# Kernel optimization log

Hardware: AMD Instinct MI355X
Metric: run time of the kernel (lower is better)

The kernel has to match this reference:

```python
import jax, jax.numpy as jnp
import numpy as np

B, T, D, O = 32, 1024, 1024, 256


def _glorot(key, shape):
    fan_in, fan_out = shape[0], shape[-1]
    std = np.sqrt(2.0 / (fan_in + fan_out))
    return jax.random.normal(key, shape, dtype=jnp.float32) * std


def setup_inputs() -> dict:
    key = jax.random.key(0)
    ks = jax.random.split(key, 14)
    return {
        "inputs": jax.random.normal(ks[0], (B, T, D), dtype=jnp.float32),
        # attention cell params
        "Wa": _glorot(ks[1], (O, O)),
        "Ua": _glorot(ks[2], (D, O)),
        "Va": _glorot(ks[3], (O, 1)),
        "Ba1": _glorot(ks[4], (1, O)),
        "Ba2": _glorot(ks[5], (T, O)),
        "Ba3": _glorot(ks[6], (T, 1)),
        # cascaded GRU cell params (Bo1 and inner keras GRUCell are unused in call)
        "Wo": _glorot(ks[7], (O, 1)),
        "Uo": _glorot(ks[8], (D, O)),
        "Co": _glorot(ks[9], (D, O)),
        "Bo2": _glorot(ks[10], (1, O)),
        "Bo3": _glorot(ks[11], (1, O)),
        "Bo4": _glorot(ks[12], (1, O)),
        "emb": _glorot(ks[13], (O, O)),
    }


def reference(inputs, Wa, Ua, Va, Ba1, Ba2, Ba3, Wo, Uo, Co, Bo2, Bo3, Bo4, emb):
    # inputs: [B, T, D]
    # UaH is identical every decoder step in the original code -> hoist (same math).
    UaH = jnp.einsum("btd,do->bto", inputs, Ua) + Ba2          # [B,T,O]
    # prev_state at step t is inputs[:, t-1, :] with wraparound at t=0.
    prev_in = jnp.roll(inputs, 1, axis=1)                        # [B,T,D]
    UoH_all = jnp.einsum("btd,do->bto", prev_in, Uo) + Bo2      # [B,T,O]

    def step(prev_pred, uoh_t):
        # --- attention cell (query = tanh(prev_pred)) ---
        WaS = jnp.tanh(prev_pred) @ Wa + Ba1                     # [B,O]
        scores = jnp.tanh(UaH + WaS[:, None, :]) @ Va + Ba3     # [B,T,1]
        sm = jax.nn.softmax(scores, axis=1)                      # [B,T,1]
        ctx = jnp.sum(inputs * sm, axis=1)                       # [B,D]
        # --- cascaded GRU cell ---
        woy = (jax.nn.softmax(prev_pred) @ emb) @ Wo             # [B,1]
        coc = ctx @ Co + Bo3                                     # [B,O]
        pred = woy + uoh_t + coc + Bo4                           # [B,O]
        return pred, pred

    init = jnp.zeros((inputs.shape[0], Wa.shape[0]), dtype=inputs.dtype)
    _, outs = jax.lax.scan(step, init, jnp.swapaxes(UoH_all, 0, 1))  # [T,B,O]
    return jnp.swapaxes(outs, 0, 1)                                   # [B,T,O]
```

## Files before the change

### kernel.cpp

```cpp
#include <hip/hip_runtime.h>
#include <hip/hip_fp16.h>


typedef unsigned int uint32;
typedef unsigned short u16;

#define NTH 512

__device__ __forceinline__ float b2f(u16 u) { return __uint_as_float(((uint32)u) << 16); }
__device__ __forceinline__ u16 f2b(float f) {
    uint32 u = __float_as_uint(f);
    uint32 r = u + 0x7fffu + ((u >> 16) & 1u);
    return (u16)(r >> 16);
}
__device__ __forceinline__ float lo_bf(uint32 d) { return __uint_as_float(d << 16); }
__device__ __forceinline__ float hi_bf(uint32 d) { return __uint_as_float(d & 0xffff0000u); }
__device__ __forceinline__ float tanh_fast(float x) {
    float e = __expf(x + x);
    return 1.0f - 2.0f * __builtin_amdgcn_rcpf(e + 1.0f);
}
__device__ __forceinline__ uint32 packh(float f, int t) {
    return (((uint32)t) << 16) | (uint32)__half_as_ushort(__float2half(f));
}
__device__ __forceinline__ float unpackh(uint32 w) {
    return __half2float(__ushort_as_half((unsigned short)(w & 0xFFFFu)));
}

#define OFF_E  ((size_t)0)
#define OFF_IC ((size_t)16777216)
#define WS_NEEDED ((size_t)33554432)

__device__ uint32 g_P[2][32][2064];
__device__ float g_embWo[256];

__global__ __launch_bounds__(256) void init_k() {
    int i = blockIdx.x * 256 + threadIdx.x;
    ((uint32*)g_P)[i] = 0xFFFF0000u;
}

__global__ void setup_embWo(const float* __restrict__ emb, const float* __restrict__ Wo) {
    int o = threadIdx.x;
    float a = 0.f;
    for (int j = 0; j < 256; j++) a = fmaf(emb[o * 256 + j], Wo[j], a);
    g_embWo[o] = a;
}

__global__ __launch_bounds__(256) void gemm_pre(
    const float* __restrict__ in, const float* __restrict__ Ua,
    const float* __restrict__ Uo, const float* __restrict__ Co,
    const float* __restrict__ Ba2, const float* __restrict__ Bo2,
    const float* __restrict__ Bo3, const float* __restrict__ Bo4,
    u16* __restrict__ E, float* __restrict__ outStage, u16* __restrict__ ic) {
    __shared__ __align__(16) float smA[32][132];
    __shared__ __align__(16) float smB[32][128];

    int tid = threadIdx.x;
    int rt = blockIdx.x, ct = blockIdx.y;
    int mat = ct >> 1;
    int o0 = (ct & 1) * 128;
    const float* W = (mat == 0) ? Ua : (mat == 1 ? Uo : Co);
    int r0 = rt * 128;
    int b = r0 >> 10, t0 = r0 & 1023;
    int tr = tid >> 4, tc = tid & 15;

    float acc[8][8];
#pragma unroll
    for (int i = 0; i < 8; i++)
#pragma unroll
        for (int j = 0; j < 8; j++) acc[i][j] = 0.f;

    for (int kc = 0; kc < 1024; kc += 32) {
#pragma unroll
        for (int l = 0; l < 4; l++) {
            int s = tid + l * 256;
            int i = s >> 3, c = s & 7;
            float4 v = *(const float4*)(in + (size_t)(r0 + i) * 1024 + kc + c * 4);
            smA[c * 4 + 0][i] = v.x;
            smA[c * 4 + 1][i] = v.y;
            smA[c * 4 + 2][i] = v.z;
            smA[c * 4 + 3][i] = v.w;
        }
#pragma unroll
        for (int l = 0; l < 4; l++) {
            int s = tid + l * 256;
            int dd = s >> 5, c = s & 31;
            *(float4*)&smB[dd][c * 4] = *(const float4*)(W + (size_t)(kc + dd) * 256 + o0 + c * 4);
        }
        __syncthreads();
#pragma unroll 4
        for (int j = 0; j < 32; j++) {
            float a0[8], b0[8];
            *(float4*)&a0[0] = *(const float4*)&smA[j][tr * 8];
            *(float4*)&a0[4] = *(const float4*)&smA[j][tr * 8 + 4];
            *(float4*)&b0[0] = *(const float4*)&smB[j][tc * 8];
            *(float4*)&b0[4] = *(const float4*)&smB[j][tc * 8 + 4];
#pragma unroll
            for (int rr = 0; rr < 8; rr++)
#pragma unroll
                for (int cc = 0; cc < 8; cc++) acc[rr][cc] = fmaf(a0[rr], b0[cc], acc[rr][cc]);
        }
        __syncthreads();
    }

    if (mat == 0) {
#pragma unroll
        for (int rr = 0; rr < 8; rr++) {
            int t = t0 + tr * 8 + rr;
#pragma unroll
            for (int cc = 0; cc < 8; cc++) {
                int o = o0 + tc * 8 + cc;
                float v = __expf(2.f * (acc[rr][cc] + Ba2[t * 256 + o]));
                E[((((size_t)b << 10) + t) << 8) + o] = f2b(v);
            }
        }
    } else if (mat == 1) {
#pragma unroll
        for (int rr = 0; rr < 8; rr++) {
            int t = t0 + tr * 8 + rr;
            int t1 = (t + 1) & 1023;
#pragma unroll
            for (int cc = 0; cc < 8; cc++) {
                int o = o0 + tc * 8 + cc;
                outStage[(((size_t)b << 10) + t1) * 256 + o] = acc[rr][cc] + Bo2[o] + Bo3[o] + Bo4[o];
            }
        }
    } else {
#pragma unroll
        for (int rr = 0; rr < 8; rr++) {
            int t = t0 + tr * 8 + rr;
#pragma unroll
            for (int cc = 0; cc < 8; cc++)
                ic[(((size_t)b << 10) + t) * 256 + o0 + tc * 8 + cc] = f2b(acc[rr][cc]);
        }
    }
}

__global__ __launch_bounds__(NTH) void seq8(
    const float* __restrict__ Wa, const float* __restrict__ Va,
    const float* __restrict__ Ba1, const float* __restrict__ Ba3,
    const u16* __restrict__ E, const u16* __restrict__ IC,
    float* __restrict__ out) {
    __shared__ uint32 smWa2[128 * 256];
    __shared__ __align__(16) float smScratch[2064];
    __shared__ float smPred[256], smQ[256], smF[256], smVa[256], smBa1[256];
    __shared__ float smS[128], smEe[128], smBa3[128];
    __shared__ float smT[16];

    int tid = threadIdx.x;
    int b = blockIdx.x & 31, g = blockIdx.x >> 5;
    int lane = tid & 63, w = tid >> 6;
    int t0 = g << 7;

    if (tid < 256) {
        smVa[tid] = Va[tid]; smBa1[tid] = Ba1[tid];
        smPred[tid] = 0.f; smQ[tid] = 0.f;
    }
    if (tid < 128) smBa3[tid] = Ba3[t0 + tid];
    for (int idx = tid; idx < 32768; idx += NTH) {
        int j2 = idx >> 8, o = idx & 255;
        uint32 u0 = (uint32)f2b(Wa[(size_t)(2 * j2) * 256 + o]);
        uint32 u1 = (uint32)f2b(Wa[(size_t)(2 * j2 + 1) * 256 + o]);
        smWa2[idx] = u0 | (u1 << 16);
    }
    __syncthreads();

    float sv = (tid < 256) ? smVa[tid] : 0.f;
#pragma unroll
    for (int off = 32; off; off >>= 1) sv += __shfl_xor(sv, off, 64);
    if (lane == 0) smT[w] = sv;
    __syncthreads();
    float sumVa = smT[0] + smT[1] + smT[2] + smT[3];
    float myEmb = (tid < 256) ? g_embWo[tid] : 0.f;
    __syncthreads();

    const u16* Eb = E + ((size_t)b << 18);
    const u16* ICb = IC + ((size_t)b << 18);
    float* outb = out + ((size_t)b << 18);
    long bud = 1000000000L;

    for (int t = 0; t < 1024; t++) {
        uint32* buf = &g_P[t & 1][b][0];
        float uoh = (tid < 256) ? outb[((size_t)t << 8) + tid] : 0.f;

        float pv = 0.f;
        if (tid < 256) {
            pv = smPred[tid];
            float m = pv;
#pragma unroll
            for (int off = 32; off; off >>= 1) m = fmaxf(m, __shfl_xor(m, off, 64));
            if (lane == 0) smT[w] = m;
        }
        {
            int o = tid & 255, h = tid >> 8;
            const uint32* wp = &smWa2[(h << 6) * 256 + o];
            const float* qp = &smQ[h << 7];
            float a = 0.f;
#pragma unroll 8
            for (int j2 = 0; j2 < 64; j2++) {
                float2 q2 = *(const float2*)&qp[j2 * 2];
                uint32 p = wp[j2 << 8];
                a = fmaf(lo_bf(p), q2.x, a);
                a = fmaf(hi_bf(p), q2.y, a);
            }
            smScratch[tid] = a;
        }
        __syncthreads();
        if (tid < 256) {
            float M = fmaxf(fmaxf(smT[0], smT[1]), fmaxf(smT[2], smT[3]));
            float e = __expf(pv - M);
            float s1 = e, s2 = e * myEmb;
#pragma unroll
            for (int off = 32; off; off >>= 1) {
                s1 += __shfl_xor(s1, off, 64);
                s2 += __shfl_xor(s2, off, 64);
            }
            if (lane == 0) { smT[4 + w] = s1; smT[8 + w] = s2; }
            smF[tid] = __expf(2.f * (smBa1[tid] + smScratch[tid] + smScratch[256 + tid]));
        }
        __syncthreads();
        float p_val = (smT[8] + smT[9] + smT[10] + smT[11]) *
                      __builtin_amdgcn_rcpf(smT[4] + smT[5] + smT[6] + smT[7]);

        {
            int tl = tid >> 2, oq = tid & 3;
            const uint4* row = (const uint4*)(Eb + (((size_t)(t0 + tl)) << 8) + (oq << 6));
            float acc = 0.f;
#pragma unroll
            for (int k = 0; k < 8; k++) {
                uint4 ev = row[k];
                int ob = (oq << 6) + (k << 3);
                float4 fA = *(const float4*)&smF[ob];
                float4 fB = *(const float4*)&smF[ob + 4];
                float4 vA = *(const float4*)&smVa[ob];
                float4 vB = *(const float4*)&smVa[ob + 4];
                acc = fmaf(vA.x, __builtin_amdgcn_rcpf(fmaf(lo_bf(ev.x), fA.x, 1.f)), acc);
                acc = fmaf(vA.y, __builtin_amdgcn_rcpf(fmaf(hi_bf(ev.x), fA.y, 1.f)), acc);
                acc = fmaf(vA.z, __builtin_amdgcn_rcpf(fmaf(lo_bf(ev.y), fA.z, 1.f)), acc);
                acc = fmaf(vA.w, __builtin_amdgcn_rcpf(fmaf(hi_bf(ev.y), fA.w, 1.f)), acc);
                acc = fmaf(vB.x, __builtin_amdgcn_rcpf(fmaf(lo_bf(ev.z), fB.x, 1.f)), acc);
                acc = fmaf(vB.y, __builtin_amdgcn_rcpf(fmaf(hi_bf(ev.z), fB.y, 1.f)), acc);
                acc = fmaf(vB.z, __builtin_amdgcn_rcpf(fmaf(lo_bf(ev.w), fB.z, 1.f)), acc);
                acc = fmaf(vB.w, __builtin_amdgcn_rcpf(fmaf(hi_bf(ev.w), fB.w, 1.f)), acc);
            }
            acc += __shfl_xor(acc, 1, 64);
            acc += __shfl_xor(acc, 2, 64);
            if (oq == 0) smS[tl] = sumVa - 2.f * acc + smBa3[tl];
        }
        __syncthreads();
        float m_g = 0.f, S_g = 0.f;
        if (tid < 128) {
            float s = smS[tid];
            float mm = s;
#pragma unroll
            for (int off = 32; off; off >>= 1) mm = fmaxf(mm, __shfl_xor(mm, off, 64));
            if (lane == 0) smT[w] = mm;
        }
        __syncthreads();
        if (tid < 128) {
            m_g = fmaxf(smT[0], smT[1]);
            float e = __expf(smS[tid] - m_g);
            smEe[tid] = e;
            float ls = e;
#pragma unroll
            for (int off = 32; off; off >>= 1) ls += __shfl_xor(ls, off, 64);
            if (lane == 0) smT[2 + w] = ls;
        }
        __syncthreads();
        m_g = fmaxf(smT[0], smT[1]);
        S_g = smT[2] + smT[3];

        {
            int rg = tid >> 6, oc = tid & 63, o4 = oc << 2;
            const u16* icp = ICb + (((size_t)t0) << 8) + o4;
            float4 a4 = {0.f, 0.f, 0.f, 0.f};
#pragma unroll 4
            for (int r = 0; r < 16; r++) {
                int row = (rg << 4) + r;
                float e = smEe[row];
                uint2 iv = *(const uint2*)(icp + ((size_t)row << 8));
                a4.x = fmaf(e, lo_bf(iv.x), a4.x);
                a4.y = fmaf(e, hi_bf(iv.x), a4.y);
                a4.z = fmaf(e, lo_bf(iv.y), a4.z);
                a4.w = fmaf(e, hi_bf(iv.y), a4.w);
            }
            *(float4*)&smScratch[rg * 256 + o4] = a4;
        }
        __syncthreads();
        if (tid < 256) {
            float P = 0.f;
#pragma unroll
            for (int rg = 0; rg < 8; rg++) P += smScratch[rg * 256 + tid];
            atomicExch(&buf[g * 258 + tid], packh(P, t));
        }
        if (tid == 0) {
            atomicExch(&buf[g * 258 + 256], packh(m_g, t));
            atomicExch(&buf[g * 258 + 257], packh(S_g, t));
        }
        __syncthreads();
        {
            uint32 tt = (uint32)t;
            uint32 w0 = 0xFFFF0000u, w1 = 0xFFFF0000u, w2 = 0xFFFF0000u, w3 = 0xFFFF0000u;
            int has4 = (tid < 16);
            uint32 w4 = has4 ? 0xFFFF0000u : (tt << 16);
            while (bud > 0) {
                if ((w0 >> 16) != tt) w0 = atomicAdd(&buf[tid], 0u);
                if ((w1 >> 16) != tt) w1 = atomicAdd(&buf[tid + 512], 0u);
                if ((w2 >> 16) != tt) w2 = atomicAdd(&buf[tid + 1024], 0u);
                if ((w3 >> 16) != tt) w3 = atomicAdd(&buf[tid + 1536], 0u);
                if (has4 && (w4 >> 16) != tt) w4 = atomicAdd(&buf[tid + 2048], 0u);
                if ((w0 >> 16) == tt && (w1 >> 16) == tt && (w2 >> 16) == tt &&
                    (w3 >> 16) == tt && (w4 >> 16) == tt) break;
                bud--;
            }
            smScratch[tid] = unpackh(w0);
            smScratch[tid + 512] = unpackh(w1);
            smScratch[tid + 1024] = unpackh(w2);
            smScratch[tid + 1536] = unpackh(w3);
            if (has4) smScratch[tid + 2048] = unpackh(w4);
        }
        __syncthreads();
        if (tid < 256) {
            float M = smScratch[256];
#pragma unroll
            for (int g2 = 1; g2 < 8; g2++) M = fmaxf(M, smScratch[g2 * 258 + 256]);
            float L = 0.f, Pt = 0.f;
#pragma unroll
            for (int g2 = 0; g2 < 8; g2++) {
                float eg = __expf(smScratch[g2 * 258 + 256] - M);
                L = fmaf(eg, smScratch[g2 * 258 + 257], L);
                Pt = fmaf(eg, smScratch[g2 * 258 + tid], Pt);
            }
            float pr = p_val + uoh + Pt * __builtin_amdgcn_rcpf(L);
            if ((tid >> 5) == g) outb[((size_t)t << 8) + tid] = pr;
            smPred[tid] = pr;
            smQ[tid] = tanh_fast(pr);
        }
        __syncthreads();
    }
}

__global__ void zero_k(uint32* out, int n) {
    int i = blockIdx.x * 1024 + threadIdx.x;
    if (i < n) out[i] = 0;
}

extern "C" void kernel_launch(void* const* d_in, const int* in_sizes, int n_in,
                              void* d_out, int out_size, void* d_ws, size_t ws_size,
                              hipStream_t stream) {
    const float* in = (const float*)d_in[0];
    const float* Wa = (const float*)d_in[1];
    const float* Ua = (const float*)d_in[2];
    const float* Va = (const float*)d_in[3];
    const float* Ba1 = (const float*)d_in[4];
    const float* Ba2 = (const float*)d_in[5];
    const float* Ba3 = (const float*)d_in[6];
    const float* Wo = (const float*)d_in[7];
    const float* Uo = (const float*)d_in[8];
    const float* Co = (const float*)d_in[9];
    const float* Bo2 = (const float*)d_in[10];
    const float* Bo3 = (const float*)d_in[11];
    const float* Bo4 = (const float*)d_in[12];
    const float* emb = (const float*)d_in[13];
    float* out = (float*)d_out;
    char* ws = (char*)d_ws;

    if (ws_size < WS_NEEDED) {
        zero_k<<<(out_size + 1023) / 1024, 1024, 0, stream>>>((uint32*)out, out_size);
        return;
    }

    u16* E = (u16*)(ws + OFF_E);
    u16* icp = (u16*)(ws + OFF_IC);

    init_k<<<516, 256, 0, stream>>>();
    setup_embWo<<<1, 256, 0, stream>>>(emb, Wo);
    gemm_pre<<<dim3(256, 6), 256, 0, stream>>>(in, Ua, Uo, Co, Ba2, Bo2, Bo3, Bo4, E, out, icp);
    seq8<<<256, NTH, 0, stream>>>(Wa, Va, Ba1, Ba3, E, icp, out);
}
```

Before: 7.860 ms.

## Split each batch across four 1024-thread blocks and use relaxed atomic polling

Each batch row's sequential recurrence is now split across 4 cooperating blocks of 1024 threads instead of 8 blocks of 512 threads, so each block handles 256 timesteps of attention. This halves the number of partial results exchanged through global memory at every step. Publishing and polling now use relaxed agent-scope atomic loads and stores in place of atomicExch/atomicAdd read-modify-writes, and each block copies its own partial directly into shared memory instead of polling for it. Each block now does twice the per-step work, which lengthens the serial critical path inside a block.

```diff
diff --git a/kernel.cpp b/kernel.cpp
--- a/kernel.cpp
+++ b/kernel.cpp
@@ -5,7 +5,7 @@
 typedef unsigned int uint32;
 typedef unsigned short u16;
 
-#define NTH 512
+#define NTH 1024
 
 __device__ __forceinline__ float b2f(u16 u) { return __uint_as_float(((uint32)u) << 16); }
 __device__ __forceinline__ u16 f2b(float f) {
@@ -25,12 +25,20 @@
 __device__ __forceinline__ float unpackh(uint32 w) {
     return __half2float(__ushort_as_half((unsigned short)(w & 0xFFFFu)));
 }
+__device__ __forceinline__ float hround(float x) { return __half2float(__float2half(x)); }
+
+__device__ __forceinline__ uint32 poll_ld(uint32* p) {
+    return __hip_atomic_load(p, __ATOMIC_RELAXED, __HIP_MEMORY_SCOPE_AGENT);
+}
+__device__ __forceinline__ void pub_st(uint32* p, uint32 v) {
+    __hip_atomic_store(p, v, __ATOMIC_RELAXED, __HIP_MEMORY_SCOPE_AGENT);
+}
 
 #define OFF_E  ((size_t)0)
 #define OFF_IC ((size_t)16777216)
 #define WS_NEEDED ((size_t)33554432)
 
-__device__ uint32 g_P[2][32][2064];
+__device__ uint32 g_P[2][32][1032];
 __device__ float g_embWo[256];
 
 __global__ __launch_bounds__(256) void init_k() {
@@ -135,27 +143,27 @@
     }
 }
 
-__global__ __launch_bounds__(NTH) void seq8(
+__global__ __launch_bounds__(NTH) void seq4(
     const float* __restrict__ Wa, const float* __restrict__ Va,
     const float* __restrict__ Ba1, const float* __restrict__ Ba3,
     const u16* __restrict__ E, const u16* __restrict__ IC,
     float* __restrict__ out) {
     __shared__ uint32 smWa2[128 * 256];
-    __shared__ __align__(16) float smScratch[2064];
+    __shared__ __align__(16) float smScratch[4096];
     __shared__ float smPred[256], smQ[256], smF[256], smVa[256], smBa1[256];
-    __shared__ float smS[128], smEe[128], smBa3[128];
+    __shared__ float smS[256], smEe[256], smBa3[256];
     __shared__ float smT[16];
 
     int tid = threadIdx.x;
     int b = blockIdx.x & 31, g = blockIdx.x >> 5;
     int lane = tid & 63, w = tid >> 6;
-    int t0 = g << 7;
+    int t0 = g << 8;
 
     if (tid < 256) {
         smVa[tid] = Va[tid]; smBa1[tid] = Ba1[tid];
         smPred[tid] = 0.f; smQ[tid] = 0.f;
-    }
-    if (tid < 128) smBa3[tid] = Ba3[t0 + tid];
+        smBa3[tid] = Ba3[t0 + tid];
+    }
     for (int idx = tid; idx < 32768; idx += NTH) {
         int j2 = idx >> 8, o = idx & 255;
         uint32 u0 = (uint32)f2b(Wa[(size_t)(2 * j2) * 256 + o]);
@@ -176,7 +184,9 @@
     const u16* Eb = E + ((size_t)b << 18);
     const u16* ICb = IC + ((size_t)b << 18);
     float* outb = out + ((size_t)b << 18);
-    long bud = 1000000000L;
+    long bud = 100000000L;
+
+    int base = g * 258;
 
     for (int t = 0; t < 1024; t++) {
         uint32* buf = &g_P[t & 1][b][0];
@@ -192,11 +202,11 @@
         }
         {
             int o = tid & 255, h = tid >> 8;
-            const uint32* wp = &smWa2[(h << 6) * 256 + o];
-            const float* qp = &smQ[h << 7];
+            const uint32* wp = &smWa2[(h << 5) * 256 + o];
+            const float* qp = &smQ[h << 6];
             float a = 0.f;
 #pragma unroll 8
-            for (int j2 = 0; j2 < 64; j2++) {
+            for (int j2 = 0; j2 < 32; j2++) {
                 float2 q2 = *(const float2*)&qp[j2 * 2];
                 uint32 p = wp[j2 << 8];
                 a = fmaf(lo_bf(p), q2.x, a);
@@ -215,7 +225,8 @@
                 s2 += __shfl_xor(s2, off, 64);
             }
             if (lane == 0) { smT[4 + w] = s1; smT[8 + w] = s2; }
-            smF[tid] = __expf(2.f * (smBa1[tid] + smScratch[tid] + smScratch[256 + tid]));
+            smF[tid] = __expf(2.f * (smBa1[tid] + smScratch[tid] + smScratch[256 + tid] +
+                                     smScratch[512 + tid] + smScratch[768 + tid]));
         }
         __syncthreads();
         float p_val = (smT[8] + smT[9] + smT[10] + smT[11]) *
@@ -227,8 +238,9 @@
             float acc = 0.f;
 #pragma unroll
             for (int k = 0; k < 8; k++) {
-                uint4 ev = row[k];
-                int ob = (oq << 6) + (k << 3);
+                int kk = (k + oq) & 7;
+                uint4 ev = row[kk];
+                int ob = (oq << 6) + (kk << 3);
                 float4 fA = *(const float4*)&smF[ob];
                 float4 fB = *(const float4*)&smF[ob + 4];
                 float4 vA = *(const float4*)&smVa[ob];
@@ -247,8 +259,8 @@
             if (oq == 0) smS[tl] = sumVa - 2.f * acc + smBa3[tl];
         }
         __syncthreads();
-        float m_g = 0.f, S_g = 0.f;
-        if (tid < 128) {
+        float m_g, S_g;
+        if (tid < 256) {
             float s = smS[tid];
             float mm = s;
 #pragma unroll
@@ -256,18 +268,22 @@
             if (lane == 0) smT[w] = mm;
         }
         __syncthreads();
-        if (tid < 128) {
-            m_g = fmaxf(smT[0], smT[1]);
-            float e = __expf(smS[tid] - m_g);
+        if (tid < 256) {
+            float mg = fmaxf(fmaxf(smT[0], smT[1]), fmaxf(smT[2], smT[3]));
+            float e = __expf(smS[tid] - mg);
             smEe[tid] = e;
             float ls = e;
 #pragma unroll
             for (int off = 32; off; off >>= 1) ls += __shfl_xor(ls, off, 64);
-            if (lane == 0) smT[2 + w] = ls;
-        }
-        __syncthreads();
-        m_g = fmaxf(smT[0], smT[1]);
-        S_g = smT[2] + smT[3];
+            if (lane == 0) smT[4 + w] = ls;
+        }
+        __syncthreads();
+        m_g = fmaxf(fmaxf(smT[0], smT[1]), fmaxf(smT[2], smT[3]));
+        S_g = smT[4] + smT[5] + smT[6] + smT[7];
+        if (tid == 0) {
+            pub_st(&buf[base + 256], packh(m_g, t));
+            pub_st(&buf[base + 257], packh(S_g, t));
+        }
 
         {
             int rg = tid >> 6, oc = tid & 63, o4 = oc << 2;
@@ -286,52 +302,47 @@
             *(float4*)&smScratch[rg * 256 + o4] = a4;
         }
         __syncthreads();
-        if (tid < 256) {
-            float P = 0.f;
-#pragma unroll
-            for (int rg = 0; rg < 8; rg++) P += smScratch[rg * 256 + tid];
-            atomicExch(&buf[g * 258 + tid], packh(P, t));
-        }
-        if (tid == 0) {
-            atomicExch(&buf[g * 258 + 256], packh(m_g, t));
-            atomicExch(&buf[g * 258 + 257], packh(S_g, t));
+        float Pmine = 0.f;
+        if (tid < 256) {
+#pragma unroll
+            for (int rg = 0; rg < 16; rg++) Pmine += smScratch[rg * 256 + tid];
+            pub_st(&buf[base + tid], packh(Pmine, t));
         }
         __syncthreads();
         {
             uint32 tt = (uint32)t;
-            uint32 w0 = 0xFFFF0000u, w1 = 0xFFFF0000u, w2 = 0xFFFF0000u, w3 = 0xFFFF0000u;
-            int has4 = (tid < 16);
-            uint32 w4 = has4 ? 0xFFFF0000u : (tt << 16);
+            if (tid < 256) smScratch[base + tid] = hround(Pmine);
+            if (tid == 0) {
+                smScratch[base + 256] = hround(m_g);
+                smScratch[base + 257] = hround(S_g);
+            }
+            bool own0 = ((uint32)(tid - base) < 258u);
+            bool p1 = (tid < 8) && (g != 3);
+            uint32 w0 = own0 ? (tt << 16) : 0xFFFF0000u;
+            uint32 w1 = p1 ? 0xFFFF0000u : (tt << 16);
             while (bud > 0) {
-                if ((w0 >> 16) != tt) w0 = atomicAdd(&buf[tid], 0u);
-                if ((w1 >> 16) != tt) w1 = atomicAdd(&buf[tid + 512], 0u);
-                if ((w2 >> 16) != tt) w2 = atomicAdd(&buf[tid + 1024], 0u);
-                if ((w3 >> 16) != tt) w3 = atomicAdd(&buf[tid + 1536], 0u);
-                if (has4 && (w4 >> 16) != tt) w4 = atomicAdd(&buf[tid + 2048], 0u);
-                if ((w0 >> 16) == tt && (w1 >> 16) == tt && (w2 >> 16) == tt &&
-                    (w3 >> 16) == tt && (w4 >> 16) == tt) break;
+                if ((w0 >> 16) != tt) w0 = poll_ld(&buf[tid]);
+                if ((w1 >> 16) != tt) w1 = poll_ld(&buf[1024 + tid]);
+                if (((w0 >> 16) == tt) & ((w1 >> 16) == tt)) break;
                 bud--;
             }
-            smScratch[tid] = unpackh(w0);
-            smScratch[tid + 512] = unpackh(w1);
-            smScratch[tid + 1024] = unpackh(w2);
-            smScratch[tid + 1536] = unpackh(w3);
-            if (has4) smScratch[tid + 2048] = unpackh(w4);
+            if (!own0) smScratch[tid] = unpackh(w0);
+            if (p1) smScratch[1024 + tid] = unpackh(w1);
         }
         __syncthreads();
         if (tid < 256) {
             float M = smScratch[256];
 #pragma unroll
-            for (int g2 = 1; g2 < 8; g2++) M = fmaxf(M, smScratch[g2 * 258 + 256]);
+            for (int g2 = 1; g2 < 4; g2++) M = fmaxf(M, smScratch[g2 * 258 + 256]);
             float L = 0.f, Pt = 0.f;
 #pragma unroll
-            for (int g2 = 0; g2 < 8; g2++) {
+            for (int g2 = 0; g2 < 4; g2++) {
                 float eg = __expf(smScratch[g2 * 258 + 256] - M);
                 L = fmaf(eg, smScratch[g2 * 258 + 257], L);
                 Pt = fmaf(eg, smScratch[g2 * 258 + tid], Pt);
             }
             float pr = p_val + uoh + Pt * __builtin_amdgcn_rcpf(L);
-            if ((tid >> 5) == g) outb[((size_t)t << 8) + tid] = pr;
+            if ((tid >> 6) == g) outb[((size_t)t << 8) + tid] = pr;
             smPred[tid] = pr;
             smQ[tid] = tanh_fast(pr);
         }
@@ -372,8 +383,8 @@
     u16* E = (u16*)(ws + OFF_E);
     u16* icp = (u16*)(ws + OFF_IC);
 
-    init_k<<<516, 256, 0, stream>>>();
+    init_k<<<258, 256, 0, stream>>>();
     setup_embWo<<<1, 256, 0, stream>>>(emb, Wo);
     gemm_pre<<<dim3(256, 6), 256, 0, stream>>>(in, Ua, Uo, Co, Ba2, Bo2, Bo3, Bo4, E, out, icp);
-    seq8<<<256, NTH, 0, stream>>>(Wa, Va, Ba1, Ba3, E, icp, out);
-}
+    seq4<<<128, NTH, 0, stream>>>(Wa, Va, Ba1, Ba3, E, icp, out);
+}
```

Result: slower. 9.998 ms (+27.2%).

## Replace tagged per-word fp16 exchange with fp32 data plus per-group flags

Applied to the files above, without the earlier changes.

The cross-block exchange of partial softmax-context results changes protocol. Before, every word carried an fp16 value with a timestep tag, and all 512 threads polled every word. Now each group writes fp32 partials and its max/sum with coherent stores, then publishes a single per-group flag that only 8 threads poll before the partials are read back. This aims to cut the atomic polling traffic and latency in the per-step inter-block sync and removes the fp16 rounding. It relies on relaxed stores with no explicit release fence to order the data before the flag. A rotated k index in the score loop staggers shared-memory accesses across the quad lanes to reduce bank conflicts.

```diff
diff --git a/kernel.cpp b/kernel.cpp
--- a/kernel.cpp
+++ b/kernel.cpp
@@ -19,23 +19,24 @@
     float e = __expf(x + x);
     return 1.0f - 2.0f * __builtin_amdgcn_rcpf(e + 1.0f);
 }
-__device__ __forceinline__ uint32 packh(float f, int t) {
-    return (((uint32)t) << 16) | (uint32)__half_as_ushort(__float2half(f));
-}
-__device__ __forceinline__ float unpackh(uint32 w) {
-    return __half2float(__ushort_as_half((unsigned short)(w & 0xFFFFu)));
+
+__device__ __forceinline__ uint32 coh_ld(const uint32* p) {
+    return __hip_atomic_load(p, __ATOMIC_RELAXED, __HIP_MEMORY_SCOPE_AGENT);
+}
+__device__ __forceinline__ void coh_st(uint32* p, uint32 v) {
+    __hip_atomic_store(p, v, __ATOMIC_RELAXED, __HIP_MEMORY_SCOPE_AGENT);
 }
 
 #define OFF_E  ((size_t)0)
 #define OFF_IC ((size_t)16777216)
 #define WS_NEEDED ((size_t)33554432)
 
-__device__ uint32 g_P[2][32][2064];
+__device__ uint32 g_Pf[2][32][8][264];
+__device__ uint32 g_flag[2][32][8];
 __device__ float g_embWo[256];
 
-__global__ __launch_bounds__(256) void init_k() {
-    int i = blockIdx.x * 256 + threadIdx.x;
-    ((uint32*)g_P)[i] = 0xFFFF0000u;
+__global__ __launch_bounds__(512) void init_flags() {
+    ((uint32*)g_flag)[threadIdx.x] = 0xFFFFFFFFu;
 }
 
 __global__ void setup_embWo(const float* __restrict__ emb, const float* __restrict__ Wo) {
@@ -179,7 +180,8 @@
     long bud = 1000000000L;
 
     for (int t = 0; t < 1024; t++) {
-        uint32* buf = &g_P[t & 1][b][0];
+        uint32* bufP  = &g_Pf[t & 1][b][g][0];
+        uint32* flags = &g_flag[t & 1][b][0];
         float uoh = (tid < 256) ? outb[((size_t)t << 8) + tid] : 0.f;
 
         float pv = 0.f;
@@ -227,8 +229,9 @@
             float acc = 0.f;
 #pragma unroll
             for (int k = 0; k < 8; k++) {
-                uint4 ev = row[k];
-                int ob = (oq << 6) + (k << 3);
+                int kk = (k + oq) & 7;
+                uint4 ev = row[kk];
+                int ob = (oq << 6) + (kk << 3);
                 float4 fA = *(const float4*)&smF[ob];
                 float4 fB = *(const float4*)&smF[ob + 4];
                 float4 vA = *(const float4*)&smVa[ob];
@@ -268,6 +271,10 @@
         __syncthreads();
         m_g = fmaxf(smT[0], smT[1]);
         S_g = smT[2] + smT[3];
+        if (tid == 0) {
+            coh_st(&bufP[256], __float_as_uint(m_g));
+            coh_st(&bufP[257], __float_as_uint(S_g));
+        }
 
         {
             int rg = tid >> 6, oc = tid & 63, o4 = oc << 2;
@@ -287,48 +294,43 @@
         }
         __syncthreads();
         if (tid < 256) {
-            float P = 0.f;
-#pragma unroll
-            for (int rg = 0; rg < 8; rg++) P += smScratch[rg * 256 + tid];
-            atomicExch(&buf[g * 258 + tid], packh(P, t));
-        }
-        if (tid == 0) {
-            atomicExch(&buf[g * 258 + 256], packh(m_g, t));
-            atomicExch(&buf[g * 258 + 257], packh(S_g, t));
-        }
-        __syncthreads();
+            float Pmine = 0.f;
+#pragma unroll
+            for (int rg = 0; rg < 8; rg++) Pmine += smScratch[rg * 256 + tid];
+            coh_st(&bufP[tid], __float_as_uint(Pmine));
+        }
+        __syncthreads();
+        if (tid == 0) coh_st(&flags[g], (uint32)t);
+        if (tid < 8 && tid != g) {
+            while (bud > 0) {
+                if (atomicAdd(&flags[tid], 0u) == (uint32)t) break;
+                bud--;
+            }
+        }
+        __syncthreads();
+        float p8[8];
         {
-            uint32 tt = (uint32)t;
-            uint32 w0 = 0xFFFF0000u, w1 = 0xFFFF0000u, w2 = 0xFFFF0000u, w3 = 0xFFFF0000u;
-            int has4 = (tid < 16);
-            uint32 w4 = has4 ? 0xFFFF0000u : (tt << 16);
-            while (bud > 0) {
-                if ((w0 >> 16) != tt) w0 = atomicAdd(&buf[tid], 0u);
-                if ((w1 >> 16) != tt) w1 = atomicAdd(&buf[tid + 512], 0u);
-                if ((w2 >> 16) != tt) w2 = atomicAdd(&buf[tid + 1024], 0u);
-                if ((w3 >> 16) != tt) w3 = atomicAdd(&buf[tid + 1536], 0u);
-                if (has4 && (w4 >> 16) != tt) w4 = atomicAdd(&buf[tid + 2048], 0u);
-                if ((w0 >> 16) == tt && (w1 >> 16) == tt && (w2 >> 16) == tt &&
-                    (w3 >> 16) == tt && (w4 >> 16) == tt) break;
-                bud--;
-            }
-            smScratch[tid] = unpackh(w0);
-            smScratch[tid + 512] = unpackh(w1);
-            smScratch[tid + 1024] = unpackh(w2);
-            smScratch[tid + 1536] = unpackh(w3);
-            if (has4) smScratch[tid + 2048] = unpackh(w4);
+            const uint32* pb = &g_Pf[t & 1][b][0][0];
+            if (tid < 256) {
+#pragma unroll
+                for (int g2 = 0; g2 < 8; g2++)
+                    p8[g2] = __uint_as_float(coh_ld(&pb[g2 * 264 + tid]));
+            } else if (tid < 256 + 16) {
+                int i = tid & 15;
+                smT[i] = __uint_as_float(coh_ld(&pb[(i >> 1) * 264 + 256 + (i & 1)]));
+            }
         }
         __syncthreads();
         if (tid < 256) {
-            float M = smScratch[256];
-#pragma unroll
-            for (int g2 = 1; g2 < 8; g2++) M = fmaxf(M, smScratch[g2 * 258 + 256]);
+            float M = smT[0];
+#pragma unroll
+            for (int g2 = 1; g2 < 8; g2++) M = fmaxf(M, smT[2 * g2]);
             float L = 0.f, Pt = 0.f;
 #pragma unroll
             for (int g2 = 0; g2 < 8; g2++) {
-                float eg = __expf(smScratch[g2 * 258 + 256] - M);
-                L = fmaf(eg, smScratch[g2 * 258 + 257], L);
-                Pt = fmaf(eg, smScratch[g2 * 258 + tid], Pt);
+                float eg = __expf(smT[2 * g2] - M);
+                L = fmaf(eg, smT[2 * g2 + 1], L);
+                Pt = fmaf(eg, p8[g2], Pt);
             }
             float pr = p_val + uoh + Pt * __builtin_amdgcn_rcpf(L);
             if ((tid >> 5) == g) outb[((size_t)t << 8) + tid] = pr;
@@ -372,7 +374,7 @@
     u16* E = (u16*)(ws + OFF_E);
     u16* icp = (u16*)(ws + OFF_IC);
 
-    init_k<<<516, 256, 0, stream>>>();
+    init_flags<<<1, 512, 0, stream>>>();
     setup_embWo<<<1, 256, 0, stream>>>(emb, Wo);
     gemm_pre<<<dim3(256, 6), 256, 0, stream>>>(in, Ua, Uo, Co, Ba2, Bo2, Bo3, Bo4, E, out, icp);
     seq8<<<256, NTH, 0, stream>>>(Wa, Va, Ba1, Ba3, E, icp, out);
```

Result: faster. 6.948 ms (-11.6%).
